# Kernel tuning notes

Hardware: AMD Instinct MI355X
Metric: run time of the kernel (lower is better)

## Reference

```python
import jax, jax.numpy as jnp
import numpy as np

B, N, C = 4, 100000, 500
H = W = 512


def setup_inputs() -> dict:
    key = jax.random.key(0)
    k1, k2, k3, k4 = jax.random.split(key, 4)
    classifications = jax.random.uniform(k1, (B, N, C), dtype=jnp.float32)  # sigmoid-like scores in [0,1)
    regressions = jax.random.normal(k2, (B, N, 4), dtype=jnp.float32) * 0.5
    ctr = jax.random.uniform(k3, (1, N, 2), minval=0.0, maxval=float(W), dtype=jnp.float32)
    wh = jax.random.uniform(k4, (1, N, 2), minval=16.0, maxval=256.0, dtype=jnp.float32)
    anchors = jnp.concatenate([ctr - wh / 2, ctr + wh / 2], axis=-1)  # [1, N, 4] (x1,y1,x2,y2)
    imgs = jnp.zeros((B, 3, H, W), dtype=jnp.float32)  # only shape is used
    cls_thresh = jnp.float32(0.998)  # max of 500 uniforms is near 1; keeps mask sparse-ish
    regress_factor = jnp.array([0.1, 0.1, 0.2, 0.2], dtype=jnp.float32)
    return dict(imgs=imgs, classifications=classifications, regressions=regressions,
                anchors=anchors, cls_thresh=cls_thresh, regress_factor=regress_factor)


def _decode_and_clip(anchors, regressions, regress_factor, h, w):
    widths = anchors[..., 2] - anchors[..., 0]
    heights = anchors[..., 3] - anchors[..., 1]
    ctr_x = anchors[..., 0] + 0.5 * widths
    ctr_y = anchors[..., 1] + 0.5 * heights

    dx = regressions[..., 0] * regress_factor[0]
    dy = regressions[..., 1] * regress_factor[1]
    dw = regressions[..., 2] * regress_factor[2]
    dh = regressions[..., 3] * regress_factor[3]

    pred_ctr_x = ctr_x + dx * widths
    pred_ctr_y = ctr_y + dy * heights
    pred_w = jnp.exp(dw) * widths
    pred_h = jnp.exp(dh) * heights

    x1 = pred_ctr_x - 0.5 * pred_w
    y1 = pred_ctr_y - 0.5 * pred_h
    x2 = pred_ctr_x + 0.5 * pred_w
    y2 = pred_ctr_y + 0.5 * pred_h

    # clip_boxes_to_image((height, width)): x in [0,w], y in [0,h]
    x1 = jnp.clip(x1, 0.0, w)
    x2 = jnp.clip(x2, 0.0, w)
    y1 = jnp.clip(y1, 0.0, h)
    y2 = jnp.clip(y2, 0.0, h)
    return jnp.stack([x1, y1, x2, y2], axis=-1)  # [B, N, 4]


def reference(imgs, classifications, regressions, anchors, cls_thresh, regress_factor):
    _, _, h, w = imgs.shape
    # per-anchor max score + class (single pass)
    scores_all = jnp.max(classifications, axis=2)            # [B, N]
    cls_idx = jnp.argmax(classifications, axis=2)            # [B, N]
    mask = scores_all > cls_thresh.reshape(())               # [B, N] bool (stream-compaction mask)

    boxes = _decode_and_clip(anchors, regressions, regress_factor, float(h), float(w))  # [B, N, 4]

    # jit-friendly analogue of per-image boolean gather: zero out non-selected rows,
    # return mask so consumers can compact.
    boxes = boxes * mask[..., None]
    scores = scores_all * mask
    cls_idx = cls_idx * mask.astype(cls_idx.dtype)
    return boxes, cls_idx, scores, mask
```

## Files before the change

### kernel.cpp

```cpp
#include <hip/hip_runtime.h>

#define B_DIM 4
#define N_DIM 100000
#define C_DIM 500
#define TOTAL_ROWS (B_DIM * N_DIM)
#define IMG_W 512.0f
#define IMG_H 512.0f

typedef float floatx4 __attribute__((ext_vector_type(4)));


__device__ __forceinline__ void scan4(floatx4 q, int i0, float& best, int& bidx) {
    if (q.x > best) { best = q.x; bidx = i0;     }
    if (q.y > best) { best = q.y; bidx = i0 + 1; }
    if (q.z > best) { best = q.z; bidx = i0 + 2; }
    if (q.w > best) { best = q.w; bidx = i0 + 3; }
}

__global__ __launch_bounds__(256) void InferenceTransform_66202625900988_kernel(
    const float* __restrict__ cls,
    const float* __restrict__ reg,
    const float* __restrict__ anchors,
    const float* __restrict__ thresh_p,
    const float* __restrict__ rfac,
    float* __restrict__ out)
{
    const int lane          = threadIdx.x & 63;
    const int waveInBlock   = threadIdx.x >> 6;
    const int wavesPerBlock = blockDim.x >> 6;
    const int waveId        = blockIdx.x * wavesPerBlock + waveInBlock;
    const int nWaves        = gridDim.x * wavesPerBlock;

    const float thresh = thresh_p[0];
    const float rf0 = rfac[0], rf1 = rfac[1], rf2 = rfac[2], rf3 = rfac[3];

    float*       outBoxes = out;
    float*       outCls   = out + (size_t)TOTAL_ROWS * 4;
    float*       outScore = outCls + (size_t)TOTAL_ROWS;
    float*       outMask  = outScore + (size_t)TOTAL_ROWS;

    const bool tail = lane < (C_DIM / 4 - 64);

    for (int base = waveId * 2; base < TOTAL_ROWS; base += nWaves * 2) {
        const floatx4* p0 = (const floatx4*)(cls + (size_t)base * C_DIM);
        const floatx4* p1 = (const floatx4*)(cls + (size_t)(base + 1) * C_DIM);

        floatx4 q00 = __builtin_nontemporal_load(p0 + lane);
        floatx4 q10 = __builtin_nontemporal_load(p1 + lane);
        floatx4 q01 = {0,0,0,0}, q11 = {0,0,0,0};
        if (tail) {
            q01 = __builtin_nontemporal_load(p0 + lane + 64);
            q11 = __builtin_nontemporal_load(p1 + lane + 64);
        }

        float loc0 = -1.0f, loc1 = -1.0f;
        int   bidx0 = 0,    bidx1 = 0;
        scan4(q00, 4 * lane, loc0, bidx0);
        scan4(q10, 4 * lane, loc1, bidx1);
        if (tail) {
            scan4(q01, 4 * (lane + 64), loc0, bidx0);
            scan4(q11, 4 * (lane + 64), loc1, bidx1);
        }

        float w0 = loc0, w1 = loc1;
        #pragma unroll
        for (int off = 32; off > 0; off >>= 1) {
            w0 = fmaxf(w0, __shfl_xor(w0, off, 64));
            w1 = fmaxf(w1, __shfl_xor(w1, off, 64));
        }

        unsigned long long c0a = __ballot(loc0 == w0 && bidx0 < 256);
        unsigned long long c0  = c0a ? c0a : __ballot(loc0 == w0);
        unsigned long long c1a = __ballot(loc1 == w1 && bidx1 < 256);
        unsigned long long c1  = c1a ? c1a : __ballot(loc1 == w1);
        int idx0 = __shfl(bidx0, (int)__builtin_ctzll(c0), 64);
        int idx1 = __shfl(bidx1, (int)__builtin_ctzll(c1), 64);

        if (lane < 2) {
            const int   row  = base + lane;
            const float best = lane ? w1 : w0;
            const int   bidx = lane ? idx1 : idx0;

            const int n = row % N_DIM;
            float4 a = ((const float4*)anchors)[n];
            float4 r = ((const float4*)reg)[row];

            float width  = a.z - a.x;
            float height = a.w - a.y;
            float ctrx   = a.x + 0.5f * width;
            float ctry   = a.y + 0.5f * height;

            float px = ctrx + (r.x * rf0) * width;
            float py = ctry + (r.y * rf1) * height;
            float pw = expf(r.z * rf2) * width;
            float ph = expf(r.w * rf3) * height;

            float x1 = fminf(fmaxf(px - 0.5f * pw, 0.0f), IMG_W);
            float y1 = fminf(fmaxf(py - 0.5f * ph, 0.0f), IMG_H);
            float x2 = fminf(fmaxf(px + 0.5f * pw, 0.0f), IMG_W);
            float y2 = fminf(fmaxf(py + 0.5f * ph, 0.0f), IMG_H);

            const float m = (best > thresh) ? 1.0f : 0.0f;

            float4 box;
            box.x = x1 * m; box.y = y1 * m; box.z = x2 * m; box.w = y2 * m;
            ((float4*)outBoxes)[row] = box;
            outCls[row]   = m != 0.0f ? (float)bidx : 0.0f;
            outScore[row] = best * m;
            outMask[row]  = m;
        }
    }
}

extern "C" void kernel_launch(void* const* d_in, const int* in_sizes, int n_in,
                              void* d_out, int out_size, void* d_ws, size_t ws_size,
                              hipStream_t stream) {
    const float* cls     = (const float*)d_in[1];
    const float* reg     = (const float*)d_in[2];
    const float* anchors = (const float*)d_in[3];
    const float* thresh  = (const float*)d_in[4];
    const float* rfac    = (const float*)d_in[5];
    float* out = (float*)d_out;

    const int block = 256;
    const int grid  = 2048;

    InferenceTransform_66202625900988_kernel<<<grid, block, 0, stream>>>(
        cls, reg, anchors, thresh, rfac, out);
}
```

Measured before the change: 159.5 us.

## Software-pipeline row loads by prefetching next iteration's classifications, anchors, regressions

The grid-stride loop is restructured to issue the next pair of rows' classification loads, along with their anchor and regression loads, before computing the current pair's argmax and box decode. This double-buffers register data so memory latency overlaps with the reduction and shuffle work. The exp call also switches to the fast __expf intrinsic. The cost is higher register pressure and possibly lower occupancy, plus slightly less accurate exp results.

```diff
diff --git a/kernel.cpp b/kernel.cpp
--- a/kernel.cpp
+++ b/kernel.cpp
@@ -30,6 +30,7 @@
     const int wavesPerBlock = blockDim.x >> 6;
     const int waveId        = blockIdx.x * wavesPerBlock + waveInBlock;
     const int nWaves        = gridDim.x * wavesPerBlock;
+    const int stride        = nWaves * 2;
 
     const float thresh = thresh_p[0];
     const float rf0 = rfac[0], rf1 = rfac[1], rf2 = rfac[2], rf3 = rfac[3];
@@ -40,26 +41,43 @@
     float*       outMask  = outScore + (size_t)TOTAL_ROWS;
 
     const bool tail = lane < (C_DIM / 4 - 64);
+    const bool epi  = lane < 2;
 
-    for (int base = waveId * 2; base < TOTAL_ROWS; base += nWaves * 2) {
-        const floatx4* p0 = (const floatx4*)(cls + (size_t)base * C_DIM);
-        const floatx4* p1 = (const floatx4*)(cls + (size_t)(base + 1) * C_DIM);
+    #define LOAD_STAGE(b, x00, x10, x01, x11, aa, rr)                          \
+        {                                                                      \
+            const floatx4* p0 = (const floatx4*)(cls + (size_t)(b) * C_DIM);   \
+            const floatx4* p1 = (const floatx4*)(cls + (size_t)((b)+1) * C_DIM);\
+            x00 = __builtin_nontemporal_load(p0 + lane);                       \
+            x10 = __builtin_nontemporal_load(p1 + lane);                       \
+            if (tail) {                                                        \
+                x01 = __builtin_nontemporal_load(p0 + lane + 64);              \
+                x11 = __builtin_nontemporal_load(p1 + lane + 64);              \
+            }                                                                  \
+            if (epi) {                                                         \
+                int rw = (b) + lane;                                           \
+                aa = *(const floatx4*)(anchors + (size_t)(rw % N_DIM) * 4);    \
+                rr = *(const floatx4*)(reg + (size_t)rw * 4);                  \
+            }                                                                  \
+        }
 
-        floatx4 q00 = __builtin_nontemporal_load(p0 + lane);
-        floatx4 q10 = __builtin_nontemporal_load(p1 + lane);
-        floatx4 q01 = {0,0,0,0}, q11 = {0,0,0,0};
-        if (tail) {
-            q01 = __builtin_nontemporal_load(p0 + lane + 64);
-            q11 = __builtin_nontemporal_load(p1 + lane + 64);
-        }
+    int base = waveId * 2;
+    floatx4 c00, c10, c01 = {0,0,0,0}, c11 = {0,0,0,0}, ca = {0,0,0,0}, cr = {0,0,0,0};
+    LOAD_STAGE(base, c00, c10, c01, c11, ca, cr);
+
+    while (true) {
+        const int nxt = base + stride;
+        const bool has = nxt < TOTAL_ROWS;
+        floatx4 n00 = {0,0,0,0}, n10 = {0,0,0,0}, n01 = {0,0,0,0},
+                n11 = {0,0,0,0}, na = {0,0,0,0}, nr = {0,0,0,0};
+        if (has) LOAD_STAGE(nxt, n00, n10, n01, n11, na, nr);
 
         float loc0 = -1.0f, loc1 = -1.0f;
         int   bidx0 = 0,    bidx1 = 0;
-        scan4(q00, 4 * lane, loc0, bidx0);
-        scan4(q10, 4 * lane, loc1, bidx1);
+        scan4(c00, 4 * lane, loc0, bidx0);
+        scan4(c10, 4 * lane, loc1, bidx1);
         if (tail) {
-            scan4(q01, 4 * (lane + 64), loc0, bidx0);
-            scan4(q11, 4 * (lane + 64), loc1, bidx1);
+            scan4(c01, 4 * (lane + 64), loc0, bidx0);
+            scan4(c11, 4 * (lane + 64), loc1, bidx1);
         }
 
         float w0 = loc0, w1 = loc1;
@@ -76,24 +94,20 @@
         int idx0 = __shfl(bidx0, (int)__builtin_ctzll(c0), 64);
         int idx1 = __shfl(bidx1, (int)__builtin_ctzll(c1), 64);
 
-        if (lane < 2) {
+        if (epi) {
             const int   row  = base + lane;
             const float best = lane ? w1 : w0;
             const int   bidx = lane ? idx1 : idx0;
 
-            const int n = row % N_DIM;
-            float4 a = ((const float4*)anchors)[n];
-            float4 r = ((const float4*)reg)[row];
+            float width  = ca.z - ca.x;
+            float height = ca.w - ca.y;
+            float ctrx   = ca.x + 0.5f * width;
+            float ctry   = ca.y + 0.5f * height;
 
-            float width  = a.z - a.x;
-            float height = a.w - a.y;
-            float ctrx   = a.x + 0.5f * width;
-            float ctry   = a.y + 0.5f * height;
-
-            float px = ctrx + (r.x * rf0) * width;
-            float py = ctry + (r.y * rf1) * height;
-            float pw = expf(r.z * rf2) * width;
-            float ph = expf(r.w * rf3) * height;
+            float px = ctrx + (cr.x * rf0) * width;
+            float py = ctry + (cr.y * rf1) * height;
+            float pw = __expf(cr.z * rf2) * width;
+            float ph = __expf(cr.w * rf3) * height;
 
             float x1 = fminf(fmaxf(px - 0.5f * pw, 0.0f), IMG_W);
             float y1 = fminf(fmaxf(py - 0.5f * ph, 0.0f), IMG_H);
@@ -102,14 +116,19 @@
 
             const float m = (best > thresh) ? 1.0f : 0.0f;
 
-            float4 box;
+            floatx4 box;
             box.x = x1 * m; box.y = y1 * m; box.z = x2 * m; box.w = y2 * m;
-            ((float4*)outBoxes)[row] = box;
+            *(floatx4*)(outBoxes + (size_t)row * 4) = box;
             outCls[row]   = m != 0.0f ? (float)bidx : 0.0f;
             outScore[row] = best * m;
             outMask[row]  = m;
         }
+
+        if (!has) break;
+        base = nxt;
+        c00 = n00; c10 = n10; c01 = n01; c11 = n11; ca = na; cr = nr;
     }
+    #undef LOAD_STAGE
 }
 
 extern "C" void kernel_launch(void* const* d_in, const int* in_sizes, int n_in,
```

Measured after the change: 155.3 us. 1.03x faster.

## Software-pipeline row-pair loads with next-iteration prefetch and branchless tail

Applied to the files above, without the earlier changes.

Restructures the grid-stride loop so each wave prefetches the next pair of classification rows, plus the anchor and regression vectors, into registers while it reduces the current pair. This aims to hide global-memory latency in a purely bandwidth-bound argmax scan. The tail loads become unconditional by clamping the vector index, and all lanes now run the epilogue redundantly, writing duplicate rows, which removes divergence. It also switches expf to __expf. The cost is doubled register use for staging and a wasted prefetch on the last iteration.

```diff
diff --git a/kernel.cpp b/kernel.cpp
--- a/kernel.cpp
+++ b/kernel.cpp
@@ -4,6 +4,7 @@
 #define N_DIM 100000
 #define C_DIM 500
 #define TOTAL_ROWS (B_DIM * N_DIM)
+#define NBATCH (TOTAL_ROWS / 2)
 #define IMG_W 512.0f
 #define IMG_H 512.0f
 
@@ -15,6 +16,29 @@
     if (q.y > best) { best = q.y; bidx = i0 + 1; }
     if (q.z > best) { best = q.z; bidx = i0 + 2; }
     if (q.w > best) { best = q.w; bidx = i0 + 3; }
+}
+
+struct Stage {
+    floatx4 q00, q10, q01, q11;
+    floatx4 a, r;
+};
+
+__device__ __forceinline__ Stage load_stage(
+    const float* __restrict__ cls, const float* __restrict__ anchors,
+    const float* __restrict__ reg, int batch, int lane, int v1, int lidx)
+{
+    Stage s;
+    const int base = batch * 2;
+    const floatx4* p0 = (const floatx4*)(cls + (size_t)base * C_DIM);
+    const floatx4* p1 = (const floatx4*)(cls + (size_t)(base + 1) * C_DIM);
+    s.q00 = __builtin_nontemporal_load(p0 + lane);
+    s.q10 = __builtin_nontemporal_load(p1 + lane);
+    s.q01 = __builtin_nontemporal_load(p0 + v1);
+    s.q11 = __builtin_nontemporal_load(p1 + v1);
+    const int rw = base + lidx;
+    s.a = *(const floatx4*)(anchors + (size_t)(rw % N_DIM) * 4);
+    s.r = *(const floatx4*)(reg + (size_t)rw * 4);
+    return s;
 }
 
 __global__ __launch_bounds__(256) void InferenceTransform_66202625900988_kernel(
@@ -31,6 +55,9 @@
     const int waveId        = blockIdx.x * wavesPerBlock + waveInBlock;
     const int nWaves        = gridDim.x * wavesPerBlock;
 
+    const int v1   = (lane + 64 < C_DIM / 4) ? (lane + 64) : (C_DIM / 4 - 1);
+    const int lidx = (lane < 2) ? lane : 1;
+
     const float thresh = thresh_p[0];
     const float rf0 = rfac[0], rf1 = rfac[1], rf2 = rfac[2], rf3 = rfac[3];
 
@@ -39,28 +66,21 @@
     float*       outScore = outCls + (size_t)TOTAL_ROWS;
     float*       outMask  = outScore + (size_t)TOTAL_ROWS;
 
-    const bool tail = lane < (C_DIM / 4 - 64);
+    int batch = waveId;
+    Stage cur = load_stage(cls, anchors, reg, batch, lane, v1, lidx);
 
-    for (int base = waveId * 2; base < TOTAL_ROWS; base += nWaves * 2) {
-        const floatx4* p0 = (const floatx4*)(cls + (size_t)base * C_DIM);
-        const floatx4* p1 = (const floatx4*)(cls + (size_t)(base + 1) * C_DIM);
+    while (true) {
+        const int nb = batch + nWaves;
+        const int pb = (nb < NBATCH) ? nb : 0;
+        Stage nxt = load_stage(cls, anchors, reg, pb, lane, v1, lidx);
 
-        floatx4 q00 = __builtin_nontemporal_load(p0 + lane);
-        floatx4 q10 = __builtin_nontemporal_load(p1 + lane);
-        floatx4 q01 = {0,0,0,0}, q11 = {0,0,0,0};
-        if (tail) {
-            q01 = __builtin_nontemporal_load(p0 + lane + 64);
-            q11 = __builtin_nontemporal_load(p1 + lane + 64);
-        }
-
+        const int base = batch * 2;
         float loc0 = -1.0f, loc1 = -1.0f;
         int   bidx0 = 0,    bidx1 = 0;
-        scan4(q00, 4 * lane, loc0, bidx0);
-        scan4(q10, 4 * lane, loc1, bidx1);
-        if (tail) {
-            scan4(q01, 4 * (lane + 64), loc0, bidx0);
-            scan4(q11, 4 * (lane + 64), loc1, bidx1);
-        }
+        scan4(cur.q00, 4 * lane, loc0, bidx0);
+        scan4(cur.q10, 4 * lane, loc1, bidx1);
+        scan4(cur.q01, 4 * v1,   loc0, bidx0);
+        scan4(cur.q11, 4 * v1,   loc1, bidx1);
 
         float w0 = loc0, w1 = loc1;
         #pragma unroll
@@ -76,24 +96,20 @@
         int idx0 = __shfl(bidx0, (int)__builtin_ctzll(c0), 64);
         int idx1 = __shfl(bidx1, (int)__builtin_ctzll(c1), 64);
 
-        if (lane < 2) {
-            const int   row  = base + lane;
-            const float best = lane ? w1 : w0;
-            const int   bidx = lane ? idx1 : idx0;
+        {
+            const int   row  = base + lidx;
+            const float best = lidx ? w1 : w0;
+            const int   bidx = lidx ? idx1 : idx0;
 
-            const int n = row % N_DIM;
-            float4 a = ((const float4*)anchors)[n];
-            float4 r = ((const float4*)reg)[row];
+            float width  = cur.a.z - cur.a.x;
+            float height = cur.a.w - cur.a.y;
+            float ctrx   = cur.a.x + 0.5f * width;
+            float ctry   = cur.a.y + 0.5f * height;
 
-            float width  = a.z - a.x;
-            float height = a.w - a.y;
-            float ctrx   = a.x + 0.5f * width;
-            float ctry   = a.y + 0.5f * height;
-
-            float px = ctrx + (r.x * rf0) * width;
-            float py = ctry + (r.y * rf1) * height;
-            float pw = expf(r.z * rf2) * width;
-            float ph = expf(r.w * rf3) * height;
+            float px = ctrx + (cur.r.x * rf0) * width;
+            float py = ctry + (cur.r.y * rf1) * height;
+            float pw = __expf(cur.r.z * rf2) * width;
+            float ph = __expf(cur.r.w * rf3) * height;
 
             float x1 = fminf(fmaxf(px - 0.5f * pw, 0.0f), IMG_W);
             float y1 = fminf(fmaxf(py - 0.5f * ph, 0.0f), IMG_H);
@@ -102,13 +118,17 @@
 
             const float m = (best > thresh) ? 1.0f : 0.0f;
 
-            float4 box;
+            floatx4 box;
             box.x = x1 * m; box.y = y1 * m; box.z = x2 * m; box.w = y2 * m;
-            ((float4*)outBoxes)[row] = box;
+            *(floatx4*)(outBoxes + (size_t)row * 4) = box;
             outCls[row]   = m != 0.0f ? (float)bidx : 0.0f;
             outScore[row] = best * m;
             outMask[row]  = m;
         }
+
+        if (nb >= NBATCH) break;
+        batch = nb;
+        cur = nxt;
     }
 }
 
```

Result: faster. 154.5 us (-3.2%).

## Process eight rows per wave with 8-lane segments and XCD-aware block remap

Applied to the files above, without the earlier changes.

Each wave now handles eight classification rows at once, with eight lanes per row each loading 16 float4 chunks, so every lane has more loads in flight. The argmax reduction is replaced by a three-step shuffle with a tie-break on lowest index. Block IDs are remapped so that consecutive logical blocks land on the same XCD, and the grid is sized to 1250 blocks. Box decode now uses __expf and runs across eight lanes per group. Clamping the chunk index means the last lanes redundantly reload chunk 124, and the fast exponential may differ slightly in precision.

```diff
diff --git a/kernel.cpp b/kernel.cpp
--- a/kernel.cpp
+++ b/kernel.cpp
@@ -4,6 +4,7 @@
 #define N_DIM 100000
 #define C_DIM 500
 #define TOTAL_ROWS (B_DIM * N_DIM)
+#define NGROUPS (TOTAL_ROWS / 8)
 #define IMG_W 512.0f
 #define IMG_H 512.0f
 
@@ -28,8 +29,19 @@
     const int lane          = threadIdx.x & 63;
     const int waveInBlock   = threadIdx.x >> 6;
     const int wavesPerBlock = blockDim.x >> 6;
-    const int waveId        = blockIdx.x * wavesPerBlock + waveInBlock;
-    const int nWaves        = gridDim.x * wavesPerBlock;
+
+    const int nwg  = gridDim.x;
+    const int q    = nwg >> 3;
+    const int r    = nwg & 7;
+    const int xcd  = blockIdx.x & 7;
+    const int sidx = blockIdx.x >> 3;
+    const int bid  = (xcd < r ? xcd * (q + 1) : r * (q + 1) + (xcd - r) * q) + sidx;
+    const int waveId = bid * wavesPerBlock + waveInBlock;
+    const int nWaves = nwg * wavesPerBlock;
+
+    const int s  = lane & 7;
+    const int rr = lane >> 3;
+    const int lidx = (lane < 8) ? lane : 7;
 
     const float thresh = thresh_p[0];
     const float rf0 = rfac[0], rf1 = rfac[1], rf2 = rfac[2], rf3 = rfac[3];
@@ -39,76 +51,57 @@
     float*       outScore = outCls + (size_t)TOTAL_ROWS;
     float*       outMask  = outScore + (size_t)TOTAL_ROWS;
 
-    const bool tail = lane < (C_DIM / 4 - 64);
+    for (int g = waveId; g < NGROUPS; g += nWaves) {
+        const int row0 = g * 8;
+        const floatx4* rowp = (const floatx4*)(cls + (size_t)(row0 + rr) * C_DIM);
 
-    for (int base = waveId * 2; base < TOTAL_ROWS; base += nWaves * 2) {
-        const floatx4* p0 = (const floatx4*)(cls + (size_t)base * C_DIM);
-        const floatx4* p1 = (const floatx4*)(cls + (size_t)(base + 1) * C_DIM);
-
-        floatx4 q00 = __builtin_nontemporal_load(p0 + lane);
-        floatx4 q10 = __builtin_nontemporal_load(p1 + lane);
-        floatx4 q01 = {0,0,0,0}, q11 = {0,0,0,0};
-        if (tail) {
-            q01 = __builtin_nontemporal_load(p0 + lane + 64);
-            q11 = __builtin_nontemporal_load(p1 + lane + 64);
+        float best = -1.0f;
+        int   bidx = 0;
+        #pragma unroll
+        for (int i = 0; i < 16; ++i) {
+            int v = 8 * i + s;
+            v = (v > 124) ? 124 : v;
+            floatx4 qv = __builtin_nontemporal_load(rowp + v);
+            scan4(qv, 4 * v, best, bidx);
         }
 
-        float loc0 = -1.0f, loc1 = -1.0f;
-        int   bidx0 = 0,    bidx1 = 0;
-        scan4(q00, 4 * lane, loc0, bidx0);
-        scan4(q10, 4 * lane, loc1, bidx1);
-        if (tail) {
-            scan4(q01, 4 * (lane + 64), loc0, bidx0);
-            scan4(q11, 4 * (lane + 64), loc1, bidx1);
+        #pragma unroll
+        for (int off = 1; off < 8; off <<= 1) {
+            float ov = __shfl_xor(best, off, 64);
+            int   oi = __shfl_xor(bidx, off, 64);
+            if (ov > best || (ov == best && oi < bidx)) { best = ov; bidx = oi; }
         }
 
-        float w0 = loc0, w1 = loc1;
-        #pragma unroll
-        for (int off = 32; off > 0; off >>= 1) {
-            w0 = fmaxf(w0, __shfl_xor(w0, off, 64));
-            w1 = fmaxf(w1, __shfl_xor(w1, off, 64));
-        }
+        const float rbest = __shfl(best, lidx * 8, 64);
+        const int   ridx  = __shfl(bidx, lidx * 8, 64);
 
-        unsigned long long c0a = __ballot(loc0 == w0 && bidx0 < 256);
-        unsigned long long c0  = c0a ? c0a : __ballot(loc0 == w0);
-        unsigned long long c1a = __ballot(loc1 == w1 && bidx1 < 256);
-        unsigned long long c1  = c1a ? c1a : __ballot(loc1 == w1);
-        int idx0 = __shfl(bidx0, (int)__builtin_ctzll(c0), 64);
-        int idx1 = __shfl(bidx1, (int)__builtin_ctzll(c1), 64);
+        const int rowi = row0 + lidx;
+        const floatx4 a = *(const floatx4*)(anchors + (size_t)(rowi % N_DIM) * 4);
+        const floatx4 rg = *(const floatx4*)(reg + (size_t)rowi * 4);
 
-        if (lane < 2) {
-            const int   row  = base + lane;
-            const float best = lane ? w1 : w0;
-            const int   bidx = lane ? idx1 : idx0;
+        float width  = a.z - a.x;
+        float height = a.w - a.y;
+        float ctrx   = a.x + 0.5f * width;
+        float ctry   = a.y + 0.5f * height;
 
-            const int n = row % N_DIM;
-            float4 a = ((const float4*)anchors)[n];
-            float4 r = ((const float4*)reg)[row];
+        float px = ctrx + (rg.x * rf0) * width;
+        float py = ctry + (rg.y * rf1) * height;
+        float pw = __expf(rg.z * rf2) * width;
+        float ph = __expf(rg.w * rf3) * height;
 
-            float width  = a.z - a.x;
-            float height = a.w - a.y;
-            float ctrx   = a.x + 0.5f * width;
-            float ctry   = a.y + 0.5f * height;
+        float x1 = fminf(fmaxf(px - 0.5f * pw, 0.0f), IMG_W);
+        float y1 = fminf(fmaxf(py - 0.5f * ph, 0.0f), IMG_H);
+        float x2 = fminf(fmaxf(px + 0.5f * pw, 0.0f), IMG_W);
+        float y2 = fminf(fmaxf(py + 0.5f * ph, 0.0f), IMG_H);
 
-            float px = ctrx + (r.x * rf0) * width;
-            float py = ctry + (r.y * rf1) * height;
-            float pw = expf(r.z * rf2) * width;
-            float ph = expf(r.w * rf3) * height;
+        const float m = (rbest > thresh) ? 1.0f : 0.0f;
 
-            float x1 = fminf(fmaxf(px - 0.5f * pw, 0.0f), IMG_W);
-            float y1 = fminf(fmaxf(py - 0.5f * ph, 0.0f), IMG_H);
-            float x2 = fminf(fmaxf(px + 0.5f * pw, 0.0f), IMG_W);
-            float y2 = fminf(fmaxf(py + 0.5f * ph, 0.0f), IMG_H);
-
-            const float m = (best > thresh) ? 1.0f : 0.0f;
-
-            float4 box;
-            box.x = x1 * m; box.y = y1 * m; box.z = x2 * m; box.w = y2 * m;
-            ((float4*)outBoxes)[row] = box;
-            outCls[row]   = m != 0.0f ? (float)bidx : 0.0f;
-            outScore[row] = best * m;
-            outMask[row]  = m;
-        }
+        floatx4 box;
+        box.x = x1 * m; box.y = y1 * m; box.z = x2 * m; box.w = y2 * m;
+        *(floatx4*)(outBoxes + (size_t)rowi * 4) = box;
+        outCls[rowi]   = m != 0.0f ? (float)ridx : 0.0f;
+        outScore[rowi] = rbest * m;
+        outMask[rowi]  = m;
     }
 }
 
@@ -123,7 +116,7 @@
     float* out = (float*)d_out;
 
     const int block = 256;
-    const int grid  = 2048;
+    const int grid  = 1250;
 
     InferenceTransform_66202625900988_kernel<<<grid, block, 0, stream>>>(
         cls, reg, anchors, thresh, rfac, out);
```

New measurement: 194.5 us. 21.9% more time.
